# Optimization experiments

Measured on AMD Instinct MI355X. Metric: run time of the kernel, lower is better.

The kernel has to match this reference:

```python
import jax, jax.numpy as jnp
import numpy as np

B, IN, H = 4096, 1024, 2048

def setup_inputs() -> dict:
    key = jax.random.key(0)
    ks = jax.random.split(key, 7)
    sk = (1.0 / H) ** 0.5
    return {
        "x": jax.random.normal(ks[0], (B, IN), dtype=jnp.float32),
        "prev_h": jax.random.normal(ks[1], (B, H), dtype=jnp.float32),
        "prev_c": jax.random.normal(ks[2], (B, H), dtype=jnp.float32),
        "W_i": jax.random.uniform(ks[3], (H, H + IN), dtype=jnp.float32, minval=-sk, maxval=sk),
        "W_f": jax.random.uniform(ks[4], (H, H + IN), dtype=jnp.float32, minval=-sk, maxval=sk),
        "W_o": jax.random.uniform(ks[5], (H, H + IN), dtype=jnp.float32, minval=-sk, maxval=sk),
        "W_c": jax.random.uniform(ks[6], (H, H + IN), dtype=jnp.float32, minval=-sk, maxval=sk),
    }

def reference(x, prev_h, prev_c, W_i, W_f, W_o, W_c):
    # concat (h, x) along features: [B, H+IN]
    hx = jnp.concatenate([prev_h, x], axis=1)
    # stack 4 gate weights -> single GEMM: [B, H+IN] @ [H+IN, 4H]
    W = jnp.concatenate([W_i, W_f, W_o, W_c], axis=0)  # [4H, H+IN]
    gates = hx @ W.T  # [B, 4H]
    gi, gf, go, gc = jnp.split(gates, 4, axis=1)
    i = jax.nn.sigmoid(gi)
    f = jax.nn.sigmoid(gf)
    o = jax.nn.sigmoid(go)
    c_tilde = jnp.tanh(gc)
    next_c = f * prev_c + i * c_tilde
    next_h = o * jnp.tanh(next_c)
    return next_h, next_c
```

## Files before the change

kernel.cpp:

```cpp
#include <hip/hip_runtime.h>
#include <hip/hip_bf16.h>


#define BATCH 4096
#define INW   1024
#define HID   2048
#define GK    3072
#define GN    8192

typedef __attribute__((ext_vector_type(8))) short short8;
typedef __attribute__((ext_vector_type(4))) float floatx4;

__device__ __forceinline__ unsigned short f2bf(float f) {
    union { float f; unsigned u; } v; v.f = f;
    unsigned r = v.u + 0x7FFFu + ((v.u >> 16) & 1u);
    return (unsigned short)(r >> 16);
}
__device__ __forceinline__ float bf2f(unsigned short u) {
    union { unsigned u; float f; } v; v.u = ((unsigned)u) << 16;
    return v.f;
}
__device__ __forceinline__ float sigf(float x) {
    return 1.0f / (1.0f + __expf(-x));
}
__device__ __forceinline__ float tanhfast(float x) {
    float t = __expf(fminf(fmaxf(2.0f * x, -30.0f), 30.0f));
    return (t - 1.0f) / (t + 1.0f);
}

__global__ __launch_bounds__(256) void pack_all(const float4* __restrict__ ph,
                                                const float4* __restrict__ x,
                                                const float4* __restrict__ Wi,
                                                const float4* __restrict__ Wf,
                                                const float4* __restrict__ Wo,
                                                const float4* __restrict__ Wc,
                                                unsigned short* __restrict__ hx,
                                                unsigned short* __restrict__ Wb) {
    long i = (long)blockIdx.x * 256 + threadIdx.x;
    const float4* src;
    unsigned short* dst;
    if (i < 1048576L) {
        int r  = (int)(i >> 8);
        int c8 = (int)(i & 255);
        src = ph + 2 * i;
        dst = hx + (size_t)r * GK + (size_t)c8 * 8;
    } else if (i < 1572864L) {
        long j = i - 1048576L;
        int r  = (int)(j >> 7);
        int c8 = (int)(j & 127);
        src = x + 2 * j;
        dst = hx + (size_t)r * GK + HID + (size_t)c8 * 8;
    } else {
        long j = i - 1572864L;
        const float4* Wg;
        int g;
        if (j < 786432L)            { Wg = Wi; g = 0; }
        else if (j < 1572864L)      { Wg = Wf; g = 1; j -= 786432L; }
        else if (j < 2359296L)      { Wg = Wo; g = 2; j -= 1572864L; }
        else                        { Wg = Wc; g = 3; j -= 2359296L; }
        src = Wg + 2 * j;
        dst = Wb + (size_t)g * HID * GK + (size_t)j * 8;
    }
    float4 v0 = src[0];
    float4 v1 = src[1];
    unsigned short o[8];
    o[0] = f2bf(v0.x); o[1] = f2bf(v0.y); o[2] = f2bf(v0.z); o[3] = f2bf(v0.w);
    o[4] = f2bf(v1.x); o[5] = f2bf(v1.y); o[6] = f2bf(v1.z); o[7] = f2bf(v1.w);
    *(short8*)dst = *(const short8*)o;
}

__device__ __forceinline__ void gld16(const unsigned short* g, unsigned short* l) {
    __builtin_amdgcn_global_load_lds((const __attribute__((address_space(1))) unsigned int*)g,
                                     (__attribute__((address_space(3))) unsigned int*)l,
                                     16, 0, 0);
}

template<int VM> __device__ __forceinline__ void wait_vm() {
    if constexpr (VM == 8)      asm volatile("s_waitcnt vmcnt(8)" ::: "memory");
    else if constexpr (VM == 4) asm volatile("s_waitcnt vmcnt(4)" ::: "memory");
    else if constexpr (VM == 0) asm volatile("s_waitcnt vmcnt(0)" ::: "memory");
}

__global__ __launch_bounds__(512, 2) void gemm_bt(const unsigned short* __restrict__ A,
                                                  const unsigned short* __restrict__ Bt,
                                                  unsigned short* __restrict__ C) {
    __shared__ unsigned short lds[65536];
    const int tid  = threadIdx.x;
    const int wave = tid >> 6;
    const int lane = tid & 63;

    const int bid = blockIdx.x;
    const int swz = ((bid & 7) << 6) + (bid >> 3);
    const long row0 = (long)(swz >> 5) * 256;
    const long col0 = (long)(swz & 31) * 256;

    const int wm = wave >> 2;
    const int wn = wave & 3;

    const int c0 = ((tid & 3) - ((tid >> 3) & 3)) & 3;
    const unsigned short* gA0 = A  + (row0 + (tid >> 2)) * GK + c0 * 8;
    const unsigned short* gB0 = Bt + (col0 + (tid >> 2)) * GK + c0 * 8;

#define STAGE_A(kt, b) do { \
        unsigned short* _d = &lds[(b) * 8192 + tid * 8]; \
        gld16(gA0 + (size_t)(kt) * 32, _d); \
        gld16(gA0 + 128 * GK + (size_t)(kt) * 32, _d + 4096); \
    } while (0)
#define STAGE_B(kt, b) do { \
        unsigned short* _d = &lds[32768 + (b) * 8192 + tid * 8]; \
        gld16(gB0 + (size_t)(kt) * 32, _d); \
        gld16(gB0 + 128 * GK + (size_t)(kt) * 32, _d + 4096); \
    } while (0)

    const int fr = lane & 15;
    const int cq = lane >> 4;
    const int slot = ((cq + (fr >> 1)) & 3) << 3;
    const int aoff = (wm * 128 + fr) * 32 + slot;
    const int boff = (wn * 64 + fr) * 32 + slot;

    floatx4 acc[8][4];
    #pragma unroll
    for (int i = 0; i < 8; i++)
        #pragma unroll
        for (int j = 0; j < 4; j++)
            acc[i][j] = (floatx4)(0.0f);

    STAGE_A(0, 0); STAGE_B(0, 0);
    STAGE_A(1, 1); STAGE_B(1, 1);
    STAGE_A(2, 2); STAGE_B(2, 2);
    asm volatile("s_waitcnt vmcnt(8)" ::: "memory");
    __builtin_amdgcn_s_barrier();

#define K_ITER(t, VMW, STG) do { \
        const unsigned short* bufA = &lds[((t) & 3) * 8192]; \
        const unsigned short* bufB = &lds[32768 + ((t) & 3) * 8192]; \
        short8 af[4], bfv[4]; \
         \
        _Pragma("unroll") \
        for (int i = 0; i < 4; i++) af[i]  = *(const short8*)&bufA[aoff + i * 512]; \
        _Pragma("unroll") \
        for (int j = 0; j < 4; j++) bfv[j] = *(const short8*)&bufB[boff + j * 512]; \
        if (STG) { STAGE_A((t) + 3, ((t) + 3) & 3); } \
        __builtin_amdgcn_s_barrier(); \
        asm volatile("s_waitcnt lgkmcnt(0)" ::: "memory"); \
        __builtin_amdgcn_sched_barrier(0); \
        __builtin_amdgcn_s_setprio(1); \
        _Pragma("unroll") \
        for (int i = 0; i < 4; i++) \
            _Pragma("unroll") \
            for (int j = 0; j < 4; j++) \
                acc[i][j] = __builtin_amdgcn_mfma_f32_16x16x32_bf16(af[i], bfv[j], acc[i][j], 0, 0, 0); \
        __builtin_amdgcn_s_setprio(0); \
        __builtin_amdgcn_s_barrier(); \
         \
        _Pragma("unroll") \
        for (int i = 0; i < 4; i++) af[i] = *(const short8*)&bufA[aoff + 2048 + i * 512]; \
        if (STG) { STAGE_B((t) + 3, ((t) + 3) & 3); } \
        __builtin_amdgcn_s_barrier(); \
        asm volatile("s_waitcnt lgkmcnt(0)" ::: "memory"); \
        __builtin_amdgcn_sched_barrier(0); \
        __builtin_amdgcn_s_setprio(1); \
        _Pragma("unroll") \
        for (int i = 0; i < 4; i++) \
            _Pragma("unroll") \
            for (int j = 0; j < 4; j++) \
                acc[4 + i][j] = __builtin_amdgcn_mfma_f32_16x16x32_bf16(af[i], bfv[j], acc[4 + i][j], 0, 0, 0); \
        __builtin_amdgcn_s_setprio(0); \
        wait_vm<VMW>(); \
        __builtin_amdgcn_s_barrier(); \
    } while (0)

    int t = 0;
    for (; t < 93; ++t) K_ITER(t, 8, true);
    K_ITER(93, 4, false);
    K_ITER(94, 0, false);
    K_ITER(95, -1, false);

#undef K_ITER
#undef STAGE_A
#undef STAGE_B

    const int cr = (lane >> 4) << 2;
    const int cc = lane & 15;
    #pragma unroll
    for (int mi = 0; mi < 8; mi++) {
        #pragma unroll
        for (int nj = 0; nj < 4; nj++) {
            long base = (row0 + wm * 128 + mi * 16 + cr) * (long)GN + col0 + wn * 64 + nj * 16 + cc;
            #pragma unroll
            for (int r = 0; r < 4; r++)
                C[base + (long)r * GN] = f2bf(acc[mi][nj][r]);
        }
    }
}

__global__ __launch_bounds__(256) void lstm_ep(const unsigned short* __restrict__ gates,
                                               const float* __restrict__ prev_c,
                                               float* __restrict__ out) {
    const int i = blockIdx.x * 256 + threadIdx.x;
    const int b = i >> 9;
    const int h = (i & 511) << 2;
    const size_t gb = (size_t)b * GN + h;
    ushort4 gi = *(const ushort4*)&gates[gb];
    ushort4 gf = *(const ushort4*)&gates[gb + HID];
    ushort4 go = *(const ushort4*)&gates[gb + 2 * HID];
    ushort4 gc = *(const ushort4*)&gates[gb + 3 * HID];
    const size_t ob = (size_t)b * HID + h;
    float4 c4 = *(const float4*)&prev_c[ob];

    unsigned short giv[4] = {gi.x, gi.y, gi.z, gi.w};
    unsigned short gfv[4] = {gf.x, gf.y, gf.z, gf.w};
    unsigned short gov[4] = {go.x, go.y, go.z, go.w};
    unsigned short gcv[4] = {gc.x, gc.y, gc.z, gc.w};
    float cv[4] = {c4.x, c4.y, c4.z, c4.w};
    float nh[4], nc[4];
    #pragma unroll
    for (int j = 0; j < 4; j++) {
        float vi = sigf(bf2f(giv[j]));
        float vf = sigf(bf2f(gfv[j]));
        float vo = sigf(bf2f(gov[j]));
        float vc = tanhfast(bf2f(gcv[j]));
        float ncf = vf * cv[j] + vi * vc;
        float nhf = vo * tanhfast(ncf);
        nc[j] = ncf;
        nh[j] = nhf;
    }
    float4 vh = {nh[0], nh[1], nh[2], nh[3]};
    float4 vc4 = {nc[0], nc[1], nc[2], nc[3]};
    *(float4*)&out[ob] = vh;
    *(float4*)&out[(size_t)BATCH * HID + ob] = vc4;
}

extern "C" void kernel_launch(void* const* d_in, const int* in_sizes, int n_in,
                              void* d_out, int out_size, void* d_ws, size_t ws_size,
                              hipStream_t stream) {
    const float* x   = (const float*)d_in[0];
    const float* ph  = (const float*)d_in[1];
    const float* pc  = (const float*)d_in[2];
    const float* Wi  = (const float*)d_in[3];
    const float* Wf  = (const float*)d_in[4];
    const float* Wo  = (const float*)d_in[5];
    const float* Wc  = (const float*)d_in[6];

    unsigned short* hx    = (unsigned short*)d_ws;
    unsigned short* Wb    = hx + (size_t)BATCH * GK;
    unsigned short* gates = Wb + (size_t)GN * GK;
    float* out = (float*)d_out;

    pack_all<<<18432, 256, 0, stream>>>((const float4*)ph, (const float4*)x,
                                        (const float4*)Wi, (const float4*)Wf,
                                        (const float4*)Wo, (const float4*)Wc,
                                        hx, Wb);

    gemm_bt<<<512, 512, 0, stream>>>(hx, Wb, gates);

    lstm_ep<<<(BATCH * HID / 4) / 256, 256, 0, stream>>>(gates, pc, out);
}
```

Measured before the change: 408.2 us.

## Fuse LSTM epilogue into GEMM via gate-interleaved weight layout

The weight pack now interleaves the four gate rows per hidden unit, so each 16-column MFMA tile holds i/f/o/c for the same hidden indices. The GEMM epilogue applies the activations, swaps gate values across neighbouring lanes with shuffles, computes next_c and next_h in-register, stages them through LDS and writes coalesced float outputs. This removes the bf16 gates round trip through global memory and the separate epilogue launch. It also merges the two half-iteration barriers into one, issuing both stage loads and the second A-fragment read early, and changes the block-to-tile swizzle. The price is more register pressure and scattered prev_c loads inside the GEMM epilogue.

```diff
diff --git a/kernel.cpp b/kernel.cpp
--- a/kernel.cpp
+++ b/kernel.cpp
@@ -15,10 +15,6 @@
     union { float f; unsigned u; } v; v.f = f;
     unsigned r = v.u + 0x7FFFu + ((v.u >> 16) & 1u);
     return (unsigned short)(r >> 16);
-}
-__device__ __forceinline__ float bf2f(unsigned short u) {
-    union { unsigned u; float f; } v; v.u = ((unsigned)u) << 16;
-    return v.f;
 }
 __device__ __forceinline__ float sigf(float x) {
     return 1.0f / (1.0f + __expf(-x));
@@ -59,7 +55,9 @@
         else if (j < 2359296L)      { Wg = Wo; g = 2; j -= 1572864L; }
         else                        { Wg = Wc; g = 3; j -= 2359296L; }
         src = Wg + 2 * j;
-        dst = Wb + (size_t)g * HID * GK + (size_t)j * 8;
+        int h  = (int)(j / 384);
+        int kc = (int)(j - (long)h * 384);
+        dst = Wb + (size_t)(4 * h + g) * GK + (size_t)kc * 8;
     }
     float4 v0 = src[0];
     float4 v1 = src[1];
@@ -81,18 +79,21 @@
     else if constexpr (VM == 0) asm volatile("s_waitcnt vmcnt(0)" ::: "memory");
 }
 
-__global__ __launch_bounds__(512, 2) void gemm_bt(const unsigned short* __restrict__ A,
-                                                  const unsigned short* __restrict__ Bt,
-                                                  unsigned short* __restrict__ C) {
+__global__ __launch_bounds__(512, 2) void gemm_fused(const unsigned short* __restrict__ A,
+                                                     const unsigned short* __restrict__ Bt,
+                                                     const float* __restrict__ prev_c,
+                                                     float* __restrict__ out) {
     __shared__ unsigned short lds[65536];
     const int tid  = threadIdx.x;
     const int wave = tid >> 6;
     const int lane = tid & 63;
 
     const int bid = blockIdx.x;
-    const int swz = ((bid & 7) << 6) + (bid >> 3);
-    const long row0 = (long)(swz >> 5) * 256;
-    const long col0 = (long)(swz & 31) * 256;
+    const int x = bid & 7, ii = bid >> 3;
+    const int mt = ((x & 3) << 2) + (ii & 3);
+    const int nt = ((x >> 2) << 4) + (ii >> 2);
+    const long row0 = (long)mt * 256;
+    const long col0 = (long)nt * 256;
 
     const int wm = wave >> 2;
     const int wn = wave & 3;
@@ -134,15 +135,17 @@
 #define K_ITER(t, VMW, STG) do { \
         const unsigned short* bufA = &lds[((t) & 3) * 8192]; \
         const unsigned short* bufB = &lds[32768 + ((t) & 3) * 8192]; \
-        short8 af[4], bfv[4]; \
-         \
+        short8 af[4], af2[4], bfv[4]; \
         _Pragma("unroll") \
         for (int i = 0; i < 4; i++) af[i]  = *(const short8*)&bufA[aoff + i * 512]; \
         _Pragma("unroll") \
         for (int j = 0; j < 4; j++) bfv[j] = *(const short8*)&bufB[boff + j * 512]; \
-        if (STG) { STAGE_A((t) + 3, ((t) + 3) & 3); } \
+        __builtin_amdgcn_sched_barrier(0);  \
+        _Pragma("unroll") \
+        for (int i = 0; i < 4; i++) af2[i] = *(const short8*)&bufA[aoff + 2048 + i * 512]; \
+        if (STG) { STAGE_A((t) + 3, ((t) + 3) & 3); STAGE_B((t) + 3, ((t) + 3) & 3); } \
         __builtin_amdgcn_s_barrier(); \
-        asm volatile("s_waitcnt lgkmcnt(0)" ::: "memory"); \
+        asm volatile("s_waitcnt lgkmcnt(4)" ::: "memory"); \
         __builtin_amdgcn_sched_barrier(0); \
         __builtin_amdgcn_s_setprio(1); \
         _Pragma("unroll") \
@@ -151,12 +154,6 @@
             for (int j = 0; j < 4; j++) \
                 acc[i][j] = __builtin_amdgcn_mfma_f32_16x16x32_bf16(af[i], bfv[j], acc[i][j], 0, 0, 0); \
         __builtin_amdgcn_s_setprio(0); \
-        __builtin_amdgcn_s_barrier(); \
-         \
-        _Pragma("unroll") \
-        for (int i = 0; i < 4; i++) af[i] = *(const short8*)&bufA[aoff + 2048 + i * 512]; \
-        if (STG) { STAGE_B((t) + 3, ((t) + 3) & 3); } \
-        __builtin_amdgcn_s_barrier(); \
         asm volatile("s_waitcnt lgkmcnt(0)" ::: "memory"); \
         __builtin_amdgcn_sched_barrier(0); \
         __builtin_amdgcn_s_setprio(1); \
@@ -164,7 +161,7 @@
         for (int i = 0; i < 4; i++) \
             _Pragma("unroll") \
             for (int j = 0; j < 4; j++) \
-                acc[4 + i][j] = __builtin_amdgcn_mfma_f32_16x16x32_bf16(af[i], bfv[j], acc[4 + i][j], 0, 0, 0); \
+                acc[4 + i][j] = __builtin_amdgcn_mfma_f32_16x16x32_bf16(af2[i], bfv[j], acc[4 + i][j], 0, 0, 0); \
         __builtin_amdgcn_s_setprio(0); \
         wait_vm<VMW>(); \
         __builtin_amdgcn_s_barrier(); \
@@ -182,53 +179,48 @@
 
     const int cr = (lane >> 4) << 2;
     const int cc = lane & 15;
+    const int g  = lane & 3;
+    float* nhl = (float*)lds;
+    float* ncl = nhl + 16384;
+    const long hbase = col0 >> 2;
+
     #pragma unroll
     for (int mi = 0; mi < 8; mi++) {
         #pragma unroll
         for (int nj = 0; nj < 4; nj++) {
-            long base = (row0 + wm * 128 + mi * 16 + cr) * (long)GN + col0 + wn * 64 + nj * 16 + cc;
             #pragma unroll
-            for (int r = 0; r < 4; r++)
-                C[base + (long)r * GN] = f2bf(acc[mi][nj][r]);
+            for (int r = 0; r < 4; r++) {
+                const int row_loc = wm * 128 + mi * 16 + cr + r;
+                const int h_loc   = wn * 16 + nj * 4 + (cc >> 2);
+                float v   = acc[mi][nj][r];
+                float act = (g == 3) ? tanhfast(v) : sigf(v);
+                float t1 = __shfl_xor(act, 1);
+                float t2 = __shfl_xor(act, 2);
+                float t3 = __shfl_xor(act, 3);
+                float iv = (g == 0) ? act : (g == 1) ? t1 : (g == 2) ? t2 : t3;
+                float fv = (g == 0) ? t1 : (g == 1) ? act : (g == 2) ? t3 : t2;
+                float ov = (g == 0) ? t2 : (g == 1) ? t3 : (g == 2) ? act : t1;
+                float cv = (g == 0) ? t3 : (g == 1) ? t2 : (g == 2) ? t1 : act;
+                float pc = prev_c[(row0 + row_loc) * (long)HID + hbase + h_loc];
+                float nc = fv * pc + iv * cv;
+                float nh = ov * tanhfast(nc);
+                if (g == 0)      nhl[row_loc * 64 + h_loc] = nh;
+                else if (g == 1) ncl[row_loc * 64 + h_loc] = nc;
+            }
         }
     }
-}
-
-__global__ __launch_bounds__(256) void lstm_ep(const unsigned short* __restrict__ gates,
-                                               const float* __restrict__ prev_c,
-                                               float* __restrict__ out) {
-    const int i = blockIdx.x * 256 + threadIdx.x;
-    const int b = i >> 9;
-    const int h = (i & 511) << 2;
-    const size_t gb = (size_t)b * GN + h;
-    ushort4 gi = *(const ushort4*)&gates[gb];
-    ushort4 gf = *(const ushort4*)&gates[gb + HID];
-    ushort4 go = *(const ushort4*)&gates[gb + 2 * HID];
-    ushort4 gc = *(const ushort4*)&gates[gb + 3 * HID];
-    const size_t ob = (size_t)b * HID + h;
-    float4 c4 = *(const float4*)&prev_c[ob];
-
-    unsigned short giv[4] = {gi.x, gi.y, gi.z, gi.w};
-    unsigned short gfv[4] = {gf.x, gf.y, gf.z, gf.w};
-    unsigned short gov[4] = {go.x, go.y, go.z, go.w};
-    unsigned short gcv[4] = {gc.x, gc.y, gc.z, gc.w};
-    float cv[4] = {c4.x, c4.y, c4.z, c4.w};
-    float nh[4], nc[4];
+    __syncthreads();
+
     #pragma unroll
-    for (int j = 0; j < 4; j++) {
-        float vi = sigf(bf2f(giv[j]));
-        float vf = sigf(bf2f(gfv[j]));
-        float vo = sigf(bf2f(gov[j]));
-        float vc = tanhfast(bf2f(gcv[j]));
-        float ncf = vf * cv[j] + vi * vc;
-        float nhf = vo * tanhfast(ncf);
-        nc[j] = ncf;
-        nh[j] = nhf;
+    for (int p = 0; p < 8; p++) {
+        const int idx = p * 512 + tid;
+        const int row_loc = idx >> 4;
+        const int h4 = (idx & 15) << 2;
+        float4 vh = *(float4*)&nhl[row_loc * 64 + h4];
+        float4 vc = *(float4*)&ncl[row_loc * 64 + h4];
+        *(float4*)&out[(row0 + row_loc) * (long)HID + hbase + h4] = vh;
+        *(float4*)&out[(size_t)BATCH * HID + (row0 + row_loc) * (long)HID + hbase + h4] = vc;
     }
-    float4 vh = {nh[0], nh[1], nh[2], nh[3]};
-    float4 vc4 = {nc[0], nc[1], nc[2], nc[3]};
-    *(float4*)&out[ob] = vh;
-    *(float4*)&out[(size_t)BATCH * HID + ob] = vc4;
 }
 
 extern "C" void kernel_launch(void* const* d_in, const int* in_sizes, int n_in,
@@ -242,9 +234,8 @@
     const float* Wo  = (const float*)d_in[5];
     const float* Wc  = (const float*)d_in[6];
 
-    unsigned short* hx    = (unsigned short*)d_ws;
-    unsigned short* Wb    = hx + (size_t)BATCH * GK;
-    unsigned short* gates = Wb + (size_t)GN * GK;
+    unsigned short* hx = (unsigned short*)d_ws;
+    unsigned short* Wb = hx + (size_t)BATCH * GK;
     float* out = (float*)d_out;
 
     pack_all<<<18432, 256, 0, stream>>>((const float4*)ph, (const float4*)x,
@@ -252,7 +243,5 @@
                                         (const float4*)Wo, (const float4*)Wc,
                                         hx, Wb);
 
-    gemm_bt<<<512, 512, 0, stream>>>(hx, Wb, gates);
-
-    lstm_ep<<<(BATCH * HID / 4) / 256, 256, 0, stream>>>(gates, pc, out);
-}
+    gemm_fused<<<512, 512, 0, stream>>>(hx, Wb, pc, out);
+}
```

After: 468.1 us. +14.7%, slower.
